# Optimization experiments

Measured on AMD Instinct MI355X. Metric: run time of the kernel, lower is better.

Reference implementation:

```python
import jax, jax.numpy as jnp
import numpy as np

H = 12  # num_heads


def rotate_half(x):
    x1, x2 = jnp.split(x, 2, axis=-1)
    return jnp.concatenate([-x2, x1], axis=-1)


def setup_inputs() -> dict:
    key = jax.random.key(0)
    ks = jax.random.split(key, 8)
    B, N, C = 4, 2048, 768
    num_special = 5
    Ns = N - num_special
    D = C // H
    x = jax.random.normal(ks[0], (B, N, C), dtype=jnp.float32)
    rope_cos = jax.random.uniform(ks[1], (Ns, D), dtype=jnp.float32)
    rope_sin = jax.random.uniform(ks[2], (Ns, D), dtype=jnp.float32)
    W_qkv = jax.random.normal(ks[3], (C, 3 * C), dtype=jnp.float32) * (C ** -0.5)
    b_qkv = jax.random.normal(ks[4], (3 * C,), dtype=jnp.float32) * 0.02
    W_proj = jax.random.normal(ks[5], (C, C), dtype=jnp.float32) * (C ** -0.5)
    b_proj = jax.random.normal(ks[6], (C,), dtype=jnp.float32) * 0.02
    return {"x": x, "rope_cos": rope_cos, "rope_sin": rope_sin,
            "W_qkv": W_qkv, "b_qkv": b_qkv, "W_proj": W_proj, "b_proj": b_proj,
            "num_special": num_special}


def reference(x, rope_cos, rope_sin, W_qkv, b_qkv, W_proj, b_proj, num_special):
    B, N, C = x.shape
    D = C // H
    scale = D ** -0.5
    qkv = (x @ W_qkv + b_qkv).reshape(B, N, 3, H, D)
    qkv = jnp.transpose(qkv, (2, 0, 3, 1, 4))  # [3, B, H, N, D]
    q, k, v = qkv[0], qkv[1], qkv[2]
    # partial RoPE: special tokens untouched, spatial tokens rotated
    q_spec, q_spat = q[:, :, :num_special], q[:, :, num_special:]
    k_spec, k_spat = k[:, :, :num_special], k[:, :, num_special:]
    q_spat = q_spat * rope_cos + rotate_half(q_spat) * rope_sin
    k_spat = k_spat * rope_cos + rotate_half(k_spat) * rope_sin
    q = jnp.concatenate([q_spec, q_spat], axis=2)
    k = jnp.concatenate([k_spec, k_spat], axis=2)
    attn = jnp.einsum('bhqd,bhkd->bhqk', q, k) * scale  # [B,H,N,N]
    attn = jax.nn.softmax(attn, axis=-1)
    out = jnp.einsum('bhqk,bhkd->bhqd', attn, v)  # [B,H,N,D]
    out = jnp.transpose(out, (0, 2, 1, 3)).reshape(B, N, C)
    return out @ W_proj + b_proj
```

## Files before the change

### kernel.cpp

```cpp
#include <hip/hip_runtime.h>
#include <stdint.h>

typedef unsigned short u16;
typedef __bf16 bf16x8 __attribute__((ext_vector_type(8)));
typedef __bf16 bf16x2 __attribute__((ext_vector_type(2)));
typedef short s16x4 __attribute__((ext_vector_type(4)));
typedef float f32x4 __attribute__((ext_vector_type(4)));

typedef __attribute__((address_space(1))) void gvoid_t;
typedef __attribute__((address_space(3))) void lvoid_t;

struct alignas(16) U128 { uint32_t x, y, z, w; };
struct alignas(16) F128 { float x, y, z, w; };
struct alignas(8)  U64v { uint32_t x, y; };

__device__ __forceinline__ void gld16(const u16* g, u16* lds) {
  __builtin_amdgcn_global_load_lds((gvoid_t*)const_cast<u16*>(g),
                                   (lvoid_t*)lds, 16, 0, 0);
}

__device__ __forceinline__ u16 f2bf(float f) {
  uint32_t u = __builtin_bit_cast(uint32_t, f);
  u += 0x7FFFu + ((u >> 16) & 1u);
  return (u16)(u >> 16);
}
__device__ __forceinline__ float bf2f(u16 h) {
  return __builtin_bit_cast(float, (uint32_t)h << 16);
}
__device__ __forceinline__ bf16x8 ldfrag(const u16* p) {
  U128 u = *reinterpret_cast<const U128*>(p);
  return __builtin_bit_cast(bf16x8, u);
}
__device__ __forceinline__ uint32_t pkbf(float a, float b) {
  bf16x2 v;
  v[0] = (__bf16)a;
  v[1] = (__bf16)b;
  return __builtin_bit_cast(uint32_t, v);
}

__device__ __forceinline__ float EXP2(float x) { return __builtin_amdgcn_exp2f(x); }

__global__ void cvt_f32_bf16(const float* __restrict__ in, u16* __restrict__ out) {
  int i = (blockIdx.x * 256 + threadIdx.x) * 4;
  F128 v = *reinterpret_cast<const F128*>(in + i);
  U64v o;
  o.x = (uint32_t)f2bf(v.x) | ((uint32_t)f2bf(v.y) << 16);
  o.y = (uint32_t)f2bf(v.z) | ((uint32_t)f2bf(v.w) << 16);
  *reinterpret_cast<U64v*>(out + i) = o;
}

__global__ void transpose_cvt(const float* __restrict__ W, u16* __restrict__ Wt,
                              int K, int N) {
  __shared__ float T[32][33];
  const int n0 = blockIdx.x * 32, k0 = blockIdx.y * 32;
  const int tid = threadIdx.x;
#pragma unroll
  for (int i = 0; i < 4; ++i) {
    int e = i * 256 + tid, r = e >> 5, c = e & 31;
    T[r][c] = W[(size_t)(k0 + r) * N + n0 + c];
  }
  __syncthreads();
#pragma unroll
  for (int i = 0; i < 4; ++i) {
    int e = i * 256 + tid, r = e >> 5, c = e & 31;
    Wt[(size_t)(n0 + r) * K + k0 + c] = f2bf(T[c][r]);
  }
}

__global__ __launch_bounds__(256, 2)
void gemm_bt(const u16* __restrict__ A, const u16* __restrict__ Bt,
             const float* __restrict__ bias, float* __restrict__ C,
             int M, int N, int K) {
  __shared__ u16 As[2][128 * 32];
  __shared__ u16 Bs[2][128 * 32];
  const int tid = threadIdx.x;
  const int wave = tid >> 6, lane = tid & 63;
  const int quad = lane >> 4, l16 = lane & 15;
  const int m0 = blockIdx.y * 128, n0 = blockIdx.x * 128;
  const int wr = (wave & 1) * 64, wc = (wave >> 1) * 64;

  f32x4 acc[4][4];
#pragma unroll
  for (int i = 0; i < 4; ++i)
#pragma unroll
    for (int j = 0; j < 4; ++j) acc[i][j] = (f32x4){0.f, 0.f, 0.f, 0.f};

  const int c0 = wave * 2 * 64 + lane;
  const int row0 = c0 >> 2, kq0 = c0 & 3;
  const int c1 = c0 + 64;
  const int row1 = c1 >> 2, kq1 = c1 & 3;

#define STAGE_G(k0_, s_)                                                       \
  do {                                                                         \
    gld16(A + (size_t)(m0 + row0) * K + (k0_) + kq0 * 8, &As[s_][wave * 1024]);\
    gld16(Bt + (size_t)(n0 + row0) * K + (k0_) + kq0 * 8, &Bs[s_][wave * 1024]);\
    gld16(A + (size_t)(m0 + row1) * K + (k0_) + kq1 * 8, &As[s_][wave * 1024 + 512]); \
    gld16(Bt + (size_t)(n0 + row1) * K + (k0_) + kq1 * 8, &Bs[s_][wave * 1024 + 512]); \
  } while (0)

  STAGE_G(0, 0);
  __syncthreads();

  int cur = 0;
  for (int k0 = 0; k0 < K; k0 += 32, cur ^= 1) {
    if (k0 + 32 < K) STAGE_G(k0 + 32, cur ^ 1);
    bf16x8 af[4], bfr[4];
#pragma unroll
    for (int rb = 0; rb < 4; ++rb) af[rb] = ldfrag(&As[cur][(wr + rb * 16 + l16) * 32 + quad * 8]);
#pragma unroll
    for (int cb = 0; cb < 4; ++cb) bfr[cb] = ldfrag(&Bs[cur][(wc + cb * 16 + l16) * 32 + quad * 8]);
#pragma unroll
    for (int rb = 0; rb < 4; ++rb)
#pragma unroll
      for (int cb = 0; cb < 4; ++cb)
        acc[rb][cb] = __builtin_amdgcn_mfma_f32_16x16x32_bf16(af[rb], bfr[cb], acc[rb][cb], 0, 0, 0);
    __syncthreads();
  }
#pragma unroll
  for (int cb = 0; cb < 4; ++cb) {
    int col = n0 + wc + cb * 16 + l16;
    float bv = bias[col];
#pragma unroll
    for (int rb = 0; rb < 4; ++rb) {
#pragma unroll
      for (int r = 0; r < 4; ++r) {
        int row = m0 + wr + rb * 16 + quad * 4 + r;
        C[(size_t)row * N + col] = acc[rb][cb][r] + bv;
      }
    }
  }
#undef STAGE_G
}

__global__ __launch_bounds__(256, 2)
void gemm_qkv_rope(const u16* __restrict__ A, const u16* __restrict__ Bt,
                   const float* __restrict__ bias,
                   const float* __restrict__ cosT, const float* __restrict__ sinT,
                   const int* __restrict__ nsp,
                   u16* __restrict__ Qo, u16* __restrict__ Ko, u16* __restrict__ Vto) {
  __shared__ u16 As[2][128 * 32];
  __shared__ u16 Bs[2][128 * 32];
  const int K = 768;
  const int tid = threadIdx.x;
  const int wave = tid >> 6, lane = tid & 63;
  const int quad = lane >> 4, l16 = lane & 15;
  const int m0 = blockIdx.y * 128, n0 = blockIdx.x * 128;
  const int wr = (wave & 1) * 64, wc = (wave >> 1) * 64;

  f32x4 acc[4][4];
#pragma unroll
  for (int i = 0; i < 4; ++i)
#pragma unroll
    for (int j = 0; j < 4; ++j) acc[i][j] = (f32x4){0.f, 0.f, 0.f, 0.f};

  const int c0 = wave * 2 * 64 + lane;
  const int row0 = c0 >> 2, kq0 = c0 & 3;
  const int c1 = c0 + 64;
  const int row1 = c1 >> 2, kq1 = c1 & 3;

#define STAGE_G(k0_, s_)                                                       \
  do {                                                                         \
    gld16(A + (size_t)(m0 + row0) * K + (k0_) + kq0 * 8, &As[s_][wave * 1024]);\
    gld16(Bt + (size_t)(n0 + row0) * K + (k0_) + kq0 * 8, &Bs[s_][wave * 1024]);\
    gld16(A + (size_t)(m0 + row1) * K + (k0_) + kq1 * 8, &As[s_][wave * 1024 + 512]); \
    gld16(Bt + (size_t)(n0 + row1) * K + (k0_) + kq1 * 8, &Bs[s_][wave * 1024 + 512]); \
  } while (0)

  STAGE_G(0, 0);
  __syncthreads();

  int cur = 0;
  for (int k0 = 0; k0 < K; k0 += 32, cur ^= 1) {
    if (k0 + 32 < K) STAGE_G(k0 + 32, cur ^ 1);
    bf16x8 af[4], bfr[4];
#pragma unroll
    for (int rb = 0; rb < 4; ++rb) af[rb] = ldfrag(&As[cur][(wr + rb * 16 + l16) * 32 + quad * 8]);
#pragma unroll
    for (int cb = 0; cb < 4; ++cb) bfr[cb] = ldfrag(&Bs[cur][(wc + cb * 16 + l16) * 32 + quad * 8]);
#pragma unroll
    for (int rb = 0; rb < 4; ++rb)
#pragma unroll
      for (int cb = 0; cb < 4; ++cb)
        acc[rb][cb] = __builtin_amdgcn_mfma_f32_16x16x32_bf16(af[rb], bfr[cb], acc[rb][cb], 0, 0, 0);
    __syncthreads();
  }
#undef STAGE_G

  const int sec = blockIdx.x / 6;
  const int gcol0 = n0 + wc;
  const int hh = (gcol0 >> 6) % 12;
  const int bb = m0 >> 11;
  const int nbase = m0 & 2047;
  const int bh = bb * 12 + hh;
  const int num_special = nsp[0];
  const float QS = 0.125f * 1.4426950408889634f;

  if (sec < 2) {
    u16* outp = sec ? Ko : Qo;
    const float qs = sec ? 1.0f : QS;
#pragma unroll
    for (int cbp = 0; cbp < 2; ++cbp) {
      const int d1 = cbp * 16 + l16;
      const int d2 = d1 + 32;
      const float bv1 = bias[gcol0 + d1];
      const float bv2 = bias[gcol0 + d2];
#pragma unroll
      for (int rb = 0; rb < 4; ++rb) {
#pragma unroll
        for (int r = 0; r < 4; ++r) {
          const int n = nbase + wr + rb * 16 + quad * 4 + r;
          float v1 = acc[rb][cbp][r] + bv1;
          float v2 = acc[rb][cbp + 2][r] + bv2;
          float o1, o2;
          if (n < num_special) {
            o1 = v1; o2 = v2;
          } else {
            int ns = n - num_special;
            float c1 = cosT[ns * 64 + d1], s1 = sinT[ns * 64 + d1];
            float c2 = cosT[ns * 64 + d2], s2 = sinT[ns * 64 + d2];
            o1 = v1 * c1 - v2 * s1;
            o2 = v2 * c2 + v1 * s2;
          }
          size_t ob = ((size_t)bh * 2048 + n) * 64;
          outp[ob + d1] = f2bf(o1 * qs);
          outp[ob + d2] = f2bf(o2 * qs);
        }
      }
    }
  } else {
#pragma unroll
    for (int cb = 0; cb < 4; ++cb) {
      const int d = cb * 16 + l16;
      const float bv = bias[gcol0 + d];
#pragma unroll
      for (int rb = 0; rb < 4; ++rb) {
        const int nr = nbase + wr + rb * 16 + quad * 4;
        U64v o;
        o.x = (uint32_t)f2bf(acc[rb][cb][0] + bv) |
              ((uint32_t)f2bf(acc[rb][cb][1] + bv) << 16);
        o.y = (uint32_t)f2bf(acc[rb][cb][2] + bv) |
              ((uint32_t)f2bf(acc[rb][cb][3] + bv) << 16);
        *(U64v*)&Vto[((size_t)bh * 64 + d) * 2048 + nr] = o;
      }
    }
  }
}

__global__ __launch_bounds__(256, 3)
void attn(const u16* __restrict__ Q, const u16* __restrict__ Kg,
          const u16* __restrict__ Vt, u16* __restrict__ Out) {
  __shared__ u16 smem[2 * 8192];
  __shared__ float invS[64];
  const int tid = threadIdx.x;
  const int wave = tid >> 6, lane = tid & 63;
  const int quad = lane >> 4, l16 = lane & 15;
  const int idx = blockIdx.x;
  const int bh = idx % 48, qt = idx / 48;
  const int b = bh / 12, h = bh % 12;
  const u16* Qb = Q + (size_t)bh * 2048 * 64;
  const u16* Kb = Kg + (size_t)bh * 2048 * 64;
  const u16* Vb = Vt + (size_t)bh * 64 * 2048;
  const int wkey0 = wave * 16;

  const int lrow = lane >> 3;
  const int lch  = (lane & 7) ^ (lrow & 7);
  const int r0a = wave * 8;
  const int r0b = 32 + wave * 8;
  const int ksrc_a = (r0a + lrow) * 64 + lch * 8;
  const int ksrc_b = (r0b + lrow) * 64 + lch * 8;
  const size_t vsrc_a = (size_t)(r0a + lrow) * 2048 + lch * 8;
  const size_t vsrc_b = (size_t)(r0b + lrow) * 2048 + lch * 8;

  const int krd = (wkey0 + l16) * 64 + ((quad ^ (l16 & 7)) << 3);
  int vrd[4];
#pragma unroll
  for (int db = 0; db < 4; ++db)
    vrd[db] = (db * 16 + l16) * 64 +
              ((((wave << 1) | (quad >> 1)) ^ (l16 & 7)) << 3) + (quad & 1) * 4;

#define STAGE_A(kt_, s_)                                                      \
  do {                                                                        \
    u16* Kd = smem + (s_) * 8192;                                             \
    u16* Vd = Kd + 4096;                                                      \
    const u16* Ksrc = Kb + (size_t)(kt_) * 4096;                              \
    const u16* Vsrc = Vb + (kt_) * 64;                                        \
    gld16(Ksrc + ksrc_a, Kd + r0a * 64);                                      \
    gld16(Ksrc + ksrc_b, Kd + r0b * 64);                                      \
    gld16(Vsrc + vsrc_a, Vd + r0a * 64);                                      \
    gld16(Vsrc + vsrc_b, Vd + r0b * 64);                                      \
  } while (0)

  bf16x8 qf[4][2];
#pragma unroll
  for (int m = 0; m < 4; ++m) {
    const u16* qp = Qb + (size_t)(qt * 64 + m * 16 + l16) * 64 + quad * 8;
    qf[m][0] = ldfrag(qp);
    qf[m][1] = ldfrag(qp + 32);
  }

  f32x4 oacc[4][4];
#pragma unroll
  for (int m = 0; m < 4; ++m)
#pragma unroll
    for (int db = 0; db < 4; ++db) oacc[m][db] = (f32x4){0.f, 0.f, 0.f, 0.f};
  float psum[4] = {0.f, 0.f, 0.f, 0.f};

  STAGE_A(0, 0);
  STAGE_A(1, 1);
  __syncthreads();

  s16x4 pf[4];
  U64v  vfc[4];
  {
    const u16* Ksh = smem;
    const u16* Vsh = smem + 4096;
    bf16x8 ka0 = ldfrag(Ksh + krd);
    bf16x8 ka1 = ldfrag(Ksh + (krd ^ 32));
#pragma unroll
    for (int db = 0; db < 4; ++db) vfc[db] = *(const U64v*)(Vsh + vrd[db]);
#pragma unroll
    for (int m = 0; m < 4; ++m) {
      f32x4 st = (f32x4){0.f, 0.f, 0.f, 0.f};
      st = __builtin_amdgcn_mfma_f32_16x16x32_bf16(ka0, qf[m][0], st, 0, 0, 0);
      st = __builtin_amdgcn_mfma_f32_16x16x32_bf16(ka1, qf[m][1], st, 0, 0, 0);
      float p0 = EXP2(st[0]), p1 = EXP2(st[1]), p2 = EXP2(st[2]), p3 = EXP2(st[3]);
      psum[m] += (p0 + p1) + (p2 + p3);
      U64v pd; pd.x = pkbf(p0, p1); pd.y = pkbf(p2, p3);
      pf[m] = __builtin_bit_cast(s16x4, pd);
    }
  }
  __syncthreads();

  for (int kt = 0; kt < 31; ++kt) {
    const int cur = kt & 1, nxt = cur ^ 1;
    const u16* Kshn = smem + nxt * 8192;
    const u16* Vshn = Kshn + 4096;
    bf16x8 kn0 = ldfrag(Kshn + krd);
    bf16x8 kn1 = ldfrag(Kshn + (krd ^ 32));
    U64v vfn[4];
#pragma unroll
    for (int db = 0; db < 4; ++db) vfn[db] = *(const U64v*)(Vshn + vrd[db]);

    if (kt < 30) STAGE_A(kt + 2, cur);

    s16x4 pfn[4];
#pragma unroll
    for (int m = 0; m < 4; ++m) {
      f32x4 st = (f32x4){0.f, 0.f, 0.f, 0.f};
      st = __builtin_amdgcn_mfma_f32_16x16x32_bf16(kn0, qf[m][0], st, 0, 0, 0);
      st = __builtin_amdgcn_mfma_f32_16x16x32_bf16(kn1, qf[m][1], st, 0, 0, 0);
#pragma unroll
      for (int db = 0; db < 4; ++db)
        oacc[m][db] = __builtin_amdgcn_mfma_f32_16x16x16bf16_1k(pf[m], __builtin_bit_cast(s16x4, vfc[db]), oacc[m][db], 0, 0, 0);
      float p0 = EXP2(st[0]), p1 = EXP2(st[1]), p2 = EXP2(st[2]), p3 = EXP2(st[3]);
      psum[m] += (p0 + p1) + (p2 + p3);
      U64v pd; pd.x = pkbf(p0, p1); pd.y = pkbf(p2, p3);
      pfn[m] = __builtin_bit_cast(s16x4, pd);
    }
    __syncthreads();
#pragma unroll
    for (int m = 0; m < 4; ++m) pf[m] = pfn[m];
#pragma unroll
    for (int db = 0; db < 4; ++db) vfc[db] = vfn[db];
  }

#pragma unroll
  for (int m = 0; m < 4; ++m)
#pragma unroll
    for (int db = 0; db < 4; ++db)
      oacc[m][db] = __builtin_amdgcn_mfma_f32_16x16x16bf16_1k(pf[m], __builtin_bit_cast(s16x4, vfc[db]), oacc[m][db], 0, 0, 0);
#undef STAGE_A

#pragma unroll
  for (int m = 0; m < 4; ++m) {
    psum[m] += __shfl_xor(psum[m], 16, 64);
    psum[m] += __shfl_xor(psum[m], 32, 64);
  }
  __syncthreads();
  float* LS = (float*)smem;
  if (quad == 0) {
#pragma unroll
    for (int m = 0; m < 4; ++m) LS[wave * 64 + m * 16 + l16] = psum[m];
  }
  __syncthreads();
  if (tid < 64) {
    float tot = LS[tid] + LS[64 + tid] + LS[128 + tid] + LS[192 + tid];
    invS[tid] = 1.0f / tot;
  }

  float* OR = (float*)smem;
  const int q = tid >> 2;
  const int d0 = (tid & 3) * 4;
  const size_t obase = ((size_t)(b * 2048 + qt * 64 + q)) * 768 + h * 64 + d0;
#pragma unroll
  for (int db = 0; db < 4; ++db) {
    __syncthreads();
#pragma unroll
    for (int m = 0; m < 4; ++m)
#pragma unroll
      for (int r = 0; r < 4; ++r)
        OR[(wave * 64 + m * 16 + quad * 4 + r) * 18 + l16] = oacc[m][db][r];
    __syncthreads();
    float s0 = 0.f, s1 = 0.f, s2 = 0.f, s3 = 0.f;
#pragma unroll
    for (int w = 0; w < 4; ++w) {
      const float* p = &OR[(w * 64 + q) * 18 + d0];
      s0 += p[0]; s1 += p[1]; s2 += p[2]; s3 += p[3];
    }
    float iv = invS[q];
    U64v o;
    o.x = (uint32_t)f2bf(s0 * iv) | ((uint32_t)f2bf(s1 * iv) << 16);
    o.y = (uint32_t)f2bf(s2 * iv) | ((uint32_t)f2bf(s3 * iv) << 16);
    *(U64v*)&Out[obase + db * 16] = o;
  }
}

extern "C" void kernel_launch(void* const* d_in, const int* in_sizes, int n_in,
                              void* d_out, int out_size, void* d_ws, size_t ws_size,
                              hipStream_t stream) {
  (void)in_sizes; (void)n_in; (void)out_size; (void)ws_size;
  const float* x        = (const float*)d_in[0];
  const float* rope_cos = (const float*)d_in[1];
  const float* rope_sin = (const float*)d_in[2];
  const float* W_qkv    = (const float*)d_in[3];
  const float* b_qkv    = (const float*)d_in[4];
  const float* W_proj   = (const float*)d_in[5];
  const float* b_proj   = (const float*)d_in[6];
  const int*   nsp      = (const int*)d_in[7];
  float* out = (float*)d_out;

  char* ws = (char*)d_ws;
  u16* Xb   = (u16*)(ws);
  u16* Wqkt = (u16*)(ws + 12582912);
  u16* Wpt  = (u16*)(ws + 16121856);
  u16* Qb   = (u16*)(ws + 55050240);
  u16* Kb   = (u16*)(ws + 67633152);
  u16* Vtb  = (u16*)(ws + 80216064);
  u16* att  = (u16*)(ws + 92798976);

  cvt_f32_bf16<<<6144, 256, 0, stream>>>(x, Xb);
  transpose_cvt<<<dim3(72, 24), 256, 0, stream>>>(W_qkv, Wqkt, 768, 2304);
  transpose_cvt<<<dim3(24, 24), 256, 0, stream>>>(W_proj, Wpt, 768, 768);
  gemm_qkv_rope<<<dim3(18, 64), 256, 0, stream>>>(Xb, Wqkt, b_qkv, rope_cos, rope_sin,
                                                  nsp, Qb, Kb, Vtb);
  attn<<<1536, 256, 0, stream>>>(Qb, Kb, Vtb, att);
  gemm_bt<<<dim3(6, 64), 256, 0, stream>>>(att, Wpt, b_proj, out, 8192, 768, 768);
}
```

Baseline: 255.4 us.

## Rework both GEMMs to 128x256 tiles with triple-buffered swizzled LDS pipeline

Replaces the double-buffered 128x128, 4-wave GEMM body used by the QKV+RoPE and output projection kernels with a shared macro. The new body uses 128x256 tiles, 8 waves and a K step of 64, with a three-stage LDS ring fed by global_load_lds. Explicit vmcnt waits keep two stages in flight, an XOR swizzle reduces LDS bank conflicts, and s_setprio raises priority around the MFMA blocks. The goal is more data reuse per tile and better overlap of loads with compute. The cost is 144 KB of dynamic LDS per block, which limits occupancy to one block per CU, and the K dimension is now hard-coded to 768.

```diff
diff --git a/kernel.cpp b/kernel.cpp
--- a/kernel.cpp
+++ b/kernel.cpp
@@ -67,127 +67,101 @@
   }
 }
 
-__global__ __launch_bounds__(256, 2)
+
+#define GEMM3_BODY(A_, Bt_, K_)                                                        \
+  extern __shared__ u16 smem[];                                                        \
+  u16* Asm = smem;                               \
+  u16* Bsm = smem + 3 * 8192;                   \
+  const int tid = threadIdx.x;                                                         \
+  const int wave = tid >> 6, lane = tid & 63;                                          \
+  const int quad = lane >> 4, l16 = lane & 15;                                         \
+  const int wm = wave >> 2, wn = wave & 3;                                             \
+  const int m0 = blockIdx.y * 128, n0 = blockIdx.x * 256;                              \
+  const int lrow = lane >> 3;                                                          \
+  const int csrc = (lane & 7) ^ lrow;                   \
+  const int ar0 = wave * 16;                \
+  const int br0 = wave * 32;                \
+  const u16* Ag = (A_) + (size_t)(m0 + ar0 + lrow) * (K_) + csrc * 8;                  \
+  const u16* Bg = (Bt_) + (size_t)(n0 + br0 + lrow) * (K_) + csrc * 8;                 \
+  f32x4 acc[4][4];                                                                     \
+  _Pragma("unroll")                                                                    \
+  for (int i = 0; i < 4; ++i)                                                          \
+    _Pragma("unroll")                                                                  \
+    for (int j = 0; j < 4; ++j) acc[i][j] = (f32x4){0.f, 0.f, 0.f, 0.f};               \
+  STG3(0, 0);                                                                          \
+  STG3(1, 1);                                                                          \
+  const int arow = wm * 64 + l16;                                                      \
+  const int brow = wn * 64 + l16;                                                      \
+  const int swz = l16 & 7;                                                             \
+  for (int kt = 0; kt < 12; ++kt) {                                                    \
+    if (kt < 11) asm volatile("s_waitcnt vmcnt(6)" ::: "memory");                      \
+    else         asm volatile("s_waitcnt vmcnt(0)" ::: "memory");                      \
+    __builtin_amdgcn_s_barrier();                                                      \
+    __builtin_amdgcn_sched_barrier(0);                                                 \
+    if (kt + 2 < 12) STG3(kt + 2, (kt + 2) % 3);                                       \
+    const u16* Ab = Asm + (kt % 3) * 8192;                                             \
+    const u16* Bb = Bsm + (kt % 3) * 16384;                                            \
+    _Pragma("unroll")                                                                  \
+    for (int kk = 0; kk < 2; ++kk) {                                                   \
+      bf16x8 af[4], bfr[4];                                                            \
+      _Pragma("unroll")                                                                \
+      for (int rb = 0; rb < 4; ++rb)                                                   \
+        af[rb] = ldfrag(Ab + (arow + rb * 16) * 64 + ((((kk << 2) | quad) ^ swz) << 3)); \
+      _Pragma("unroll")                                                                \
+      for (int cb = 0; cb < 4; ++cb)                                                   \
+        bfr[cb] = ldfrag(Bb + (brow + cb * 16) * 64 + ((((kk << 2) | quad) ^ swz) << 3)); \
+      __builtin_amdgcn_s_setprio(1);                                                   \
+      _Pragma("unroll")                                                                \
+      for (int rb = 0; rb < 4; ++rb)                                                   \
+        _Pragma("unroll")                                                              \
+        for (int cb = 0; cb < 4; ++cb)                                                 \
+          acc[rb][cb] = __builtin_amdgcn_mfma_f32_16x16x32_bf16(af[rb], bfr[cb], acc[rb][cb], 0, 0, 0); \
+      __builtin_amdgcn_s_setprio(0);                                                   \
+    }                                                                                  \
+  }
+
+#define STG3(kt_, s_) do {                                                             \
+    const u16* As_ = Ag + (kt_) * 64;                                                  \
+    const u16* Bs_ = Bg + (kt_) * 64;                                                  \
+    u16* Ad = Asm + (s_) * 8192 + ar0 * 64;                                            \
+    u16* Bd = Bsm + (s_) * 16384 + br0 * 64;                                           \
+    gld16(As_, Ad);                gld16(As_ + 8 * KDIM, Ad + 512);                    \
+    gld16(Bs_, Bd);                gld16(Bs_ + 8 * KDIM, Bd + 512);                    \
+    gld16(Bs_ + 16 * KDIM, Bd + 1024); gld16(Bs_ + 24 * KDIM, Bd + 1536);              \
+  } while (0)
+
+__global__ __launch_bounds__(512, 2)
 void gemm_bt(const u16* __restrict__ A, const u16* __restrict__ Bt,
              const float* __restrict__ bias, float* __restrict__ C,
-             int M, int N, int K) {
-  __shared__ u16 As[2][128 * 32];
-  __shared__ u16 Bs[2][128 * 32];
-  const int tid = threadIdx.x;
-  const int wave = tid >> 6, lane = tid & 63;
-  const int quad = lane >> 4, l16 = lane & 15;
-  const int m0 = blockIdx.y * 128, n0 = blockIdx.x * 128;
-  const int wr = (wave & 1) * 64, wc = (wave >> 1) * 64;
-
-  f32x4 acc[4][4];
-#pragma unroll
-  for (int i = 0; i < 4; ++i)
-#pragma unroll
-    for (int j = 0; j < 4; ++j) acc[i][j] = (f32x4){0.f, 0.f, 0.f, 0.f};
-
-  const int c0 = wave * 2 * 64 + lane;
-  const int row0 = c0 >> 2, kq0 = c0 & 3;
-  const int c1 = c0 + 64;
-  const int row1 = c1 >> 2, kq1 = c1 & 3;
-
-#define STAGE_G(k0_, s_)                                                       \
-  do {                                                                         \
-    gld16(A + (size_t)(m0 + row0) * K + (k0_) + kq0 * 8, &As[s_][wave * 1024]);\
-    gld16(Bt + (size_t)(n0 + row0) * K + (k0_) + kq0 * 8, &Bs[s_][wave * 1024]);\
-    gld16(A + (size_t)(m0 + row1) * K + (k0_) + kq1 * 8, &As[s_][wave * 1024 + 512]); \
-    gld16(Bt + (size_t)(n0 + row1) * K + (k0_) + kq1 * 8, &Bs[s_][wave * 1024 + 512]); \
-  } while (0)
-
-  STAGE_G(0, 0);
-  __syncthreads();
-
-  int cur = 0;
-  for (int k0 = 0; k0 < K; k0 += 32, cur ^= 1) {
-    if (k0 + 32 < K) STAGE_G(k0 + 32, cur ^ 1);
-    bf16x8 af[4], bfr[4];
-#pragma unroll
-    for (int rb = 0; rb < 4; ++rb) af[rb] = ldfrag(&As[cur][(wr + rb * 16 + l16) * 32 + quad * 8]);
-#pragma unroll
-    for (int cb = 0; cb < 4; ++cb) bfr[cb] = ldfrag(&Bs[cur][(wc + cb * 16 + l16) * 32 + quad * 8]);
-#pragma unroll
-    for (int rb = 0; rb < 4; ++rb)
-#pragma unroll
-      for (int cb = 0; cb < 4; ++cb)
-        acc[rb][cb] = __builtin_amdgcn_mfma_f32_16x16x32_bf16(af[rb], bfr[cb], acc[rb][cb], 0, 0, 0);
-    __syncthreads();
-  }
+             int M, int N, int Karg) {
+  const int KDIM = 768;
+  (void)M; (void)Karg;
+  GEMM3_BODY(A, Bt, KDIM)
 #pragma unroll
   for (int cb = 0; cb < 4; ++cb) {
-    int col = n0 + wc + cb * 16 + l16;
+    int col = n0 + wn * 64 + cb * 16 + l16;
     float bv = bias[col];
 #pragma unroll
     for (int rb = 0; rb < 4; ++rb) {
 #pragma unroll
       for (int r = 0; r < 4; ++r) {
-        int row = m0 + wr + rb * 16 + quad * 4 + r;
+        int row = m0 + wm * 64 + rb * 16 + quad * 4 + r;
         C[(size_t)row * N + col] = acc[rb][cb][r] + bv;
       }
     }
   }
-#undef STAGE_G
-}
-
-__global__ __launch_bounds__(256, 2)
+}
+
+__global__ __launch_bounds__(512, 2)
 void gemm_qkv_rope(const u16* __restrict__ A, const u16* __restrict__ Bt,
                    const float* __restrict__ bias,
                    const float* __restrict__ cosT, const float* __restrict__ sinT,
                    const int* __restrict__ nsp,
                    u16* __restrict__ Qo, u16* __restrict__ Ko, u16* __restrict__ Vto) {
-  __shared__ u16 As[2][128 * 32];
-  __shared__ u16 Bs[2][128 * 32];
-  const int K = 768;
-  const int tid = threadIdx.x;
-  const int wave = tid >> 6, lane = tid & 63;
-  const int quad = lane >> 4, l16 = lane & 15;
-  const int m0 = blockIdx.y * 128, n0 = blockIdx.x * 128;
-  const int wr = (wave & 1) * 64, wc = (wave >> 1) * 64;
-
-  f32x4 acc[4][4];
-#pragma unroll
-  for (int i = 0; i < 4; ++i)
-#pragma unroll
-    for (int j = 0; j < 4; ++j) acc[i][j] = (f32x4){0.f, 0.f, 0.f, 0.f};
-
-  const int c0 = wave * 2 * 64 + lane;
-  const int row0 = c0 >> 2, kq0 = c0 & 3;
-  const int c1 = c0 + 64;
-  const int row1 = c1 >> 2, kq1 = c1 & 3;
-
-#define STAGE_G(k0_, s_)                                                       \
-  do {                                                                         \
-    gld16(A + (size_t)(m0 + row0) * K + (k0_) + kq0 * 8, &As[s_][wave * 1024]);\
-    gld16(Bt + (size_t)(n0 + row0) * K + (k0_) + kq0 * 8, &Bs[s_][wave * 1024]);\
-    gld16(A + (size_t)(m0 + row1) * K + (k0_) + kq1 * 8, &As[s_][wave * 1024 + 512]); \
-    gld16(Bt + (size_t)(n0 + row1) * K + (k0_) + kq1 * 8, &Bs[s_][wave * 1024 + 512]); \
-  } while (0)
-
-  STAGE_G(0, 0);
-  __syncthreads();
-
-  int cur = 0;
-  for (int k0 = 0; k0 < K; k0 += 32, cur ^= 1) {
-    if (k0 + 32 < K) STAGE_G(k0 + 32, cur ^ 1);
-    bf16x8 af[4], bfr[4];
-#pragma unroll
-    for (int rb = 0; rb < 4; ++rb) af[rb] = ldfrag(&As[cur][(wr + rb * 16 + l16) * 32 + quad * 8]);
-#pragma unroll
-    for (int cb = 0; cb < 4; ++cb) bfr[cb] = ldfrag(&Bs[cur][(wc + cb * 16 + l16) * 32 + quad * 8]);
-#pragma unroll
-    for (int rb = 0; rb < 4; ++rb)
-#pragma unroll
-      for (int cb = 0; cb < 4; ++cb)
-        acc[rb][cb] = __builtin_amdgcn_mfma_f32_16x16x32_bf16(af[rb], bfr[cb], acc[rb][cb], 0, 0, 0);
-    __syncthreads();
-  }
-#undef STAGE_G
-
-  const int sec = blockIdx.x / 6;
-  const int gcol0 = n0 + wc;
+  const int KDIM = 768;
+  GEMM3_BODY(A, Bt, KDIM)
+  const int sec = blockIdx.x / 3;
+  const int gcol0 = n0 + wn * 64;
   const int hh = (gcol0 >> 6) % 12;
   const int bb = m0 >> 11;
   const int nbase = m0 & 2047;
@@ -208,7 +182,7 @@
       for (int rb = 0; rb < 4; ++rb) {
 #pragma unroll
         for (int r = 0; r < 4; ++r) {
-          const int n = nbase + wr + rb * 16 + quad * 4 + r;
+          const int n = nbase + wm * 64 + rb * 16 + quad * 4 + r;
           float v1 = acc[rb][cbp][r] + bv1;
           float v2 = acc[rb][cbp + 2][r] + bv2;
           float o1, o2;
@@ -234,7 +208,7 @@
       const float bv = bias[gcol0 + d];
 #pragma unroll
       for (int rb = 0; rb < 4; ++rb) {
-        const int nr = nbase + wr + rb * 16 + quad * 4;
+        const int nr = nbase + wm * 64 + rb * 16 + quad * 4;
         U64v o;
         o.x = (uint32_t)f2bf(acc[rb][cb][0] + bv) |
               ((uint32_t)f2bf(acc[rb][cb][1] + bv) << 16);
@@ -438,11 +412,20 @@
   u16* Vtb  = (u16*)(ws + 80216064);
   u16* att  = (u16*)(ws + 92798976);
 
+  static bool attr_done = false;
+  if (!attr_done) {
+    hipFuncSetAttribute(reinterpret_cast<const void*>(gemm_qkv_rope),
+                        hipFuncAttributeMaxDynamicSharedMemorySize, 147456);
+    hipFuncSetAttribute(reinterpret_cast<const void*>(gemm_bt),
+                        hipFuncAttributeMaxDynamicSharedMemorySize, 147456);
+    attr_done = true;
+  }
+
   cvt_f32_bf16<<<6144, 256, 0, stream>>>(x, Xb);
   transpose_cvt<<<dim3(72, 24), 256, 0, stream>>>(W_qkv, Wqkt, 768, 2304);
   transpose_cvt<<<dim3(24, 24), 256, 0, stream>>>(W_proj, Wpt, 768, 768);
-  gemm_qkv_rope<<<dim3(18, 64), 256, 0, stream>>>(Xb, Wqkt, b_qkv, rope_cos, rope_sin,
-                                                  nsp, Qb, Kb, Vtb);
+  gemm_qkv_rope<<<dim3(9, 64), 512, 147456, stream>>>(Xb, Wqkt, b_qkv, rope_cos, rope_sin,
+                                                      nsp, Qb, Kb, Vtb);
   attn<<<1536, 256, 0, stream>>>(Qb, Kb, Vtb, att);
-  gemm_bt<<<dim3(6, 64), 256, 0, stream>>>(att, Wpt, b_proj, out, 8192, 768, 768);
-}
+  gemm_bt<<<dim3(3, 64), 512, 147456, stream>>>(att, Wpt, b_proj, out, 8192, 768, 768);
+}
```

New measurement: 261.6 us. +2.4%, slower.
